# Kernel tuning notes

Hardware: AMD Instinct MI355X
Metric: run time of the kernel (lower is better)

## Reference

```python
import jax, jax.numpy as jnp
import numpy as np

HS, FF, NH = 1024, 4096, 16
HD = HS // NH
EPS = 1e-5

def _ln(x, g, b):
    m = jnp.mean(x, axis=-1, keepdims=True)
    v = jnp.mean((x - m) ** 2, axis=-1, keepdims=True)
    return (x - m) * jax.lax.rsqrt(v + EPS) * g + b

def setup_inputs() -> dict:
    key = jax.random.key(0)
    ks = jax.random.split(key, 12)
    s = 1.0 / np.sqrt(HS)
    si = 1.0 / np.sqrt(FF)
    d = {
        "hidden_states": jax.random.normal(ks[0], (2, 2048, HS), dtype=jnp.float32),
        "attention_mask": jnp.zeros((2, 1, 1, 2048), dtype=jnp.float32),
        "Wq": jax.random.uniform(ks[1], (HS, HS), minval=-s, maxval=s),
        "bq": jnp.zeros((HS,), jnp.float32),
        "Wk": jax.random.uniform(ks[2], (HS, HS), minval=-s, maxval=s),
        "bk": jnp.zeros((HS,), jnp.float32),
        "Wv": jax.random.uniform(ks[3], (HS, HS), minval=-s, maxval=s),
        "bv": jnp.zeros((HS,), jnp.float32),
        "Wo": jax.random.uniform(ks[4], (HS, HS), minval=-s, maxval=s),
        "bo": jnp.zeros((HS,), jnp.float32),
        "W1": jax.random.uniform(ks[5], (HS, FF), minval=-s, maxval=s),
        "b1": jnp.zeros((FF,), jnp.float32),
        "W2": jax.random.uniform(ks[6], (FF, HS), minval=-si, maxval=si),
        "b2": jnp.zeros((HS,), jnp.float32),
        "ln1_g": jnp.ones((HS,), jnp.float32),
        "ln1_b": jnp.zeros((HS,), jnp.float32),
        "ln2_g": jnp.ones((HS,), jnp.float32),
        "ln2_b": jnp.zeros((HS,), jnp.float32),
    }
    return d

def reference(hidden_states, attention_mask, Wq, bq, Wk, bk, Wv, bv, Wo, bo,
              W1, b1, W2, b2, ln1_g, ln1_b, ln2_g, ln2_b):
    bs, S, _ = hidden_states.shape
    x = hidden_states
    # self-attention (dropout is identity in eval)
    q = (x @ Wq + bq).reshape(bs, S, NH, HD).transpose(0, 2, 1, 3)
    k = (x @ Wk + bk).reshape(bs, S, NH, HD).transpose(0, 2, 1, 3)
    v = (x @ Wv + bv).reshape(bs, S, NH, HD).transpose(0, 2, 1, 3)
    scores = jnp.einsum("bhqd,bhkd->bhqk", q, k) / np.sqrt(HD) + attention_mask
    probs = jax.nn.softmax(scores, axis=-1)
    attn = jnp.einsum("bhqk,bhkd->bhqd", probs, v)
    attn = attn.transpose(0, 2, 1, 3).reshape(bs, S, HS)
    mha = attn @ Wo + bo
    h = _ln(x + mha, ln1_g, ln1_b)
    # FFN
    ff = jax.nn.relu(h @ W1 + b1) @ W2 + b2
    return _ln(h + ff, ln2_g, ln2_b)
```

## Files before the change

kernel.cpp:

```cpp
#include <hip/hip_runtime.h>
#include <hip/hip_bf16.h>

#define HS   1024
#define FF   4096
#define NH   16
#define HD   64
#define SEQ  2048
#define BSZ  2
#define MROWS (BSZ * SEQ)
#define EPS  1e-5f
#define QKV_STRIDE (3 * HS)

typedef float f32x4  __attribute__((ext_vector_type(4)));
typedef short bf16x8 __attribute__((ext_vector_type(8)));

__device__ __forceinline__ unsigned short f2bf(float x) {
  unsigned int u = __float_as_uint(x);
  u += 0x7fffu + ((u >> 16) & 1u);
  return (unsigned short)(u >> 16);
}

__device__ __forceinline__ unsigned int pkbf(float a, float b) {
  union { __hip_bfloat162 h; unsigned int u; } x;
  x.h = __float22bfloat162_rn(float2{a, b});
  return x.u;
}

__device__ __forceinline__ void async16(const ushort* g, ushort* lds) {
  __builtin_amdgcn_global_load_lds(
      (const __attribute__((address_space(1))) unsigned int*)g,
      (__attribute__((address_space(3))) unsigned int*)lds, 16, 0, 0);
}

template <int TBM, int TBN, bool RELU, bool OUT_BF16>
__global__ __launch_bounds__(256) void gemm_bf16_kernel(
    const ushort* __restrict__ A, const ushort* __restrict__ Bt,
    const float* __restrict__ bias, void* __restrict__ Cout,
    int M, int N, int K)
{
  constexpr int MI = TBM / 32;
  constexpr int NJ = TBN / 32;
  __shared__ ushort As[TBM * 64];
  __shared__ ushort Bs[TBN * 64];

  const int tid = threadIdx.x;
  const int wv = tid >> 6, ln = tid & 63;
  const int bn = blockIdx.x, bm = blockIdx.y;

  const int lr = ln & 15;
  const int lg = ln >> 4;
  const int mrow_base = (wv >> 1) * (TBM / 2);
  const int ncol_base = (wv & 1) * (TBN / 2);

  f32x4 acc[MI][NJ];
#pragma unroll
  for (int i = 0; i < MI; ++i)
#pragma unroll
    for (int j = 0; j < NJ; ++j) acc[i][j] = (f32x4){0.f, 0.f, 0.f, 0.f};

  const int rr = ln >> 3, cc = ln & 7;

  for (int k0 = 0; k0 < K; k0 += 64) {
    __syncthreads();
#pragma unroll
    for (int t = 0; t < TBM / 32; ++t) {
      const int R = wv * (TBM / 4) + t * 8 + rr;
      const int c = cc ^ (R & 7);
      async16(A + (size_t)(bm * TBM + R) * K + k0 + c * 8,
              &As[(size_t)(wv * (TBM / 4) + t * 8) * 64]);
    }
#pragma unroll
    for (int t = 0; t < TBN / 32; ++t) {
      const int R = wv * (TBN / 4) + t * 8 + rr;
      const int c = cc ^ (R & 7);
      async16(Bt + (size_t)(bn * TBN + R) * K + k0 + c * 8,
              &Bs[(size_t)(wv * (TBN / 4) + t * 8) * 64]);
    }
    __syncthreads();

#pragma unroll
    for (int s = 0; s < 2; ++s) {
      bf16x8 a[MI], b[NJ];
#pragma unroll
      for (int i = 0; i < MI; ++i) {
        const int m = mrow_base + i * 16 + lr;
        a[i] = *(const bf16x8*)&As[(size_t)m * 64 + (((s * 4 + lg) ^ (m & 7)) * 8)];
      }
#pragma unroll
      for (int j = 0; j < NJ; ++j) {
        const int n = ncol_base + j * 16 + lr;
        b[j] = *(const bf16x8*)&Bs[(size_t)n * 64 + (((s * 4 + lg) ^ (n & 7)) * 8)];
      }
#pragma unroll
      for (int i = 0; i < MI; ++i)
#pragma unroll
        for (int j = 0; j < NJ; ++j)
          acc[i][j] = __builtin_amdgcn_mfma_f32_16x16x32_bf16(a[i], b[j], acc[i][j], 0, 0, 0);
    }
  }

  const int gm0 = bm * TBM + mrow_base;
  const int gn0 = bn * TBN + ncol_base;
  float bs4[NJ];
#pragma unroll
  for (int j = 0; j < NJ; ++j) bs4[j] = bias[gn0 + j * 16 + lr];

  float* Cf = (float*)Cout;
  ushort* Cb = (ushort*)Cout;
#pragma unroll
  for (int i = 0; i < MI; ++i) {
#pragma unroll
    for (int r = 0; r < 4; ++r) {
      const size_t row = (size_t)(gm0 + i * 16 + lg * 4 + r);
#pragma unroll
      for (int j = 0; j < NJ; ++j) {
        float val = acc[i][j][r] + bs4[j];
        if (RELU) val = fmaxf(val, 0.f);
        const size_t idx = row * N + gn0 + j * 16 + lr;
        if (OUT_BF16) Cb[idx] = f2bf(val);
        else          Cf[idx] = val;
      }
    }
  }
}

__global__ __launch_bounds__(256) void transpose_bf16_kernel(
    const float* __restrict__ W, ushort* __restrict__ Wt, int K, int N)
{
  __shared__ ushort T[64][72];
  const int tid = threadIdx.x;
  const int n0 = blockIdx.x * 64, k0 = blockIdx.y * 64;
#pragma unroll
  for (int t = 0; t < 4; ++t) {
    const int r = t * 16 + (tid >> 4);
    const int c = (tid & 15) * 4;
    const float4 w = *(const float4*)&W[(size_t)(k0 + r) * N + n0 + c];
    T[c + 0][r] = f2bf(w.x); T[c + 1][r] = f2bf(w.y);
    T[c + 2][r] = f2bf(w.z); T[c + 3][r] = f2bf(w.w);
  }
  __syncthreads();
#pragma unroll
  for (int t = 0; t < 4; ++t) {
    const int n = t * 16 + (tid >> 4);
    const int kc = (tid & 15) * 4;
    ushort4 o;
    o.x = T[n][kc]; o.y = T[n][kc + 1]; o.z = T[n][kc + 2]; o.w = T[n][kc + 3];
    *(ushort4*)&Wt[(size_t)(n0 + n) * K + k0 + kc] = o;
  }
}

__global__ __launch_bounds__(256) void convert_bf16_kernel(
    const float* __restrict__ X, ushort* __restrict__ Y)
{
  const size_t i = ((size_t)blockIdx.x * 256 + threadIdx.x) * 4;
  const float4 v = *(const float4*)&X[i];
  ushort4 o;
  o.x = f2bf(v.x); o.y = f2bf(v.y); o.z = f2bf(v.z); o.w = f2bf(v.w);
  *(ushort4*)&Y[i] = o;
}

__global__ __launch_bounds__(256) void biascat_kernel(
    const float* __restrict__ bq, const float* __restrict__ bk,
    const float* __restrict__ bv, float* __restrict__ bqkv)
{
  const int i = blockIdx.x * 256 + threadIdx.x;
  const float v = (i < HS) ? bq[i] : (i < 2 * HS) ? bk[i - HS] : bv[i - 2 * HS];
  bqkv[i] = v;
}

__global__ __launch_bounds__(256) void vtrans_kernel(
    const ushort* __restrict__ vb, ushort* __restrict__ VTg, int stride)
{
  __shared__ ushort T[64][68];
  const int tid = threadIdx.x;
  const int s0 = blockIdx.x * 64;
  const int bh = blockIdx.y;
  const int b = bh >> 4, h = bh & 15;
#pragma unroll
  for (int t = 0; t < 4; ++t) {
    const int rr = t * 16 + (tid >> 4);
    const int c4 = (tid & 15) * 4;
    const ushort4 w = *(const ushort4*)&vb[(size_t)(b * SEQ + s0 + rr) * stride + h * 64 + c4];
    T[c4 + 0][rr] = w.x; T[c4 + 1][rr] = w.y;
    T[c4 + 2][rr] = w.z; T[c4 + 3][rr] = w.w;
  }
  __syncthreads();
#pragma unroll
  for (int t = 0; t < 4; ++t) {
    const int d = t * 16 + (tid >> 4);
    const int k4 = (tid & 15) * 4;
    ushort4 o;
    o.x = T[d][k4]; o.y = T[d][k4 + 1]; o.z = T[d][k4 + 2]; o.w = T[d][k4 + 3];
    *(ushort4*)&VTg[((size_t)bh * 64 + d) * SEQ + s0 + k4] = o;
  }
}

__global__ __launch_bounds__(512, 4) void attention_mfma_kernel(
    const ushort* __restrict__ Qb, const ushort* __restrict__ Kb,
    const ushort* __restrict__ VTg, const float* __restrict__ mask,
    ushort* __restrict__ O)
{
  __shared__ ushort smem[16384];
  ushort* Ks  = smem;
  ushort* VTs = smem + 4096;
  ushort* Ps  = smem + 8192;

  const int tid = threadIdx.x;
  const int wv = tid >> 6, ln = tid & 63;
  const int c = ln & 15, g = ln >> 4;
  const int qt = blockIdx.x, hh = blockIdx.y, b = blockIdx.z;
  const int bh = b * NH + hh;
  const size_t row0 = (size_t)b * SEQ + (size_t)qt * 128;
  const int ch = hh * HD;
  const int wq0 = wv * 16;

  bf16x8 qf[2];
#pragma unroll
  for (int s = 0; s < 2; ++s)
    qf[s] = *(const bf16x8*)&Qb[(row0 + wq0 + c) * QKV_STRIDE + ch + s * 32 + g * 8];

  f32x4 ao[4];
#pragma unroll
  for (int i = 0; i < 4; ++i) ao[i] = (f32x4){0, 0, 0, 0};
  float m_r = -1e30f, l_r = 0.f;

  ushort* Pw = Ps + wv * 1024;
  const int rr = ln >> 3, cc = ln & 7;

  for (int kb = 0; kb < SEQ / 64; ++kb) {
    __syncthreads();
    const size_t krow0 = (size_t)b * SEQ + (size_t)kb * 64;
    if (wv < 4) {
#pragma unroll
      for (int t = 0; t < 2; ++t) {
        const int r = (wv & 3) * 16 + t * 8 + rr;
        async16(Kb + (krow0 + r) * QKV_STRIDE + ch + ((cc ^ (r & 7)) * 8),
                &Ks[(size_t)((wv & 3) * 16 + t * 8) * 64]);
      }
    } else {
#pragma unroll
      for (int t = 0; t < 2; ++t) {
        const int r = (wv & 3) * 16 + t * 8 + rr;
        async16(VTg + ((size_t)bh * 64 + r) * SEQ + kb * 64 + ((cc ^ (r & 7)) * 8),
                &VTs[(size_t)((wv & 3) * 16 + t * 8) * 64]);
      }
    }
    __syncthreads();

    f32x4 as_[4];
#pragma unroll
    for (int i = 0; i < 4; ++i) as_[i] = (f32x4){0, 0, 0, 0};
#pragma unroll
    for (int s = 0; s < 2; ++s) {
#pragma unroll
      for (int mt = 0; mt < 4; ++mt) {
        const bf16x8 kf = *(const bf16x8*)&Ks[(size_t)(mt * 16 + c) * 64 + (((s * 4 + g) ^ (c & 7)) * 8)];
        as_[mt] = __builtin_amdgcn_mfma_f32_16x16x32_bf16(kf, qf[s], as_[mt], 0, 0, 0);
      }
    }

#pragma unroll
    for (int mt = 0; mt < 4; ++mt) {
      const float4 mk = *(const float4*)&mask[(size_t)b * SEQ + kb * 64 + mt * 16 + g * 4];
      as_[mt][0] = as_[mt][0] * 0.125f + mk.x;
      as_[mt][1] = as_[mt][1] * 0.125f + mk.y;
      as_[mt][2] = as_[mt][2] * 0.125f + mk.z;
      as_[mt][3] = as_[mt][3] * 0.125f + mk.w;
    }

    {
      float mx = -1e30f;
#pragma unroll
      for (int mt = 0; mt < 4; ++mt)
#pragma unroll
        for (int r = 0; r < 4; ++r) mx = fmaxf(mx, as_[mt][r]);
      mx = fmaxf(mx, __shfl_xor(mx, 16, 64));
      mx = fmaxf(mx, __shfl_xor(mx, 32, 64));
      const float nm = fmaxf(m_r, mx);
      const float alpha = __expf(m_r - nm);
      m_r = nm;
      float sum = 0.f;
#pragma unroll
      for (int mt = 0; mt < 4; ++mt)
#pragma unroll
        for (int r = 0; r < 4; ++r) {
          const float p = __expf(as_[mt][r] - nm);
          as_[mt][r] = p;
          sum += p;
        }
      sum += __shfl_xor(sum, 16, 64);
      sum += __shfl_xor(sum, 32, 64);
      l_r = l_r * alpha + sum;
#pragma unroll
      for (int mt = 0; mt < 4; ++mt)
#pragma unroll
        for (int r = 0; r < 4; ++r) ao[mt][r] *= alpha;
    }

#pragma unroll
    for (int mt = 0; mt < 4; ++mt) {
      const int q = c;
      const int kc = 2 * mt + (g >> 1);
      const int base = q * 64 + ((kc ^ (q & 7)) * 8) + 4 * (g & 1);
      *(unsigned int*)&Pw[base]     = pkbf(as_[mt][0], as_[mt][1]);
      *(unsigned int*)&Pw[base + 2] = pkbf(as_[mt][2], as_[mt][3]);
    }

#pragma unroll
    for (int s = 0; s < 2; ++s) {
      const bf16x8 pf = *(const bf16x8*)&Pw[(size_t)c * 64 + (((s * 4 + g) ^ (c & 7)) * 8)];
#pragma unroll
      for (int mt = 0; mt < 4; ++mt) {
        const bf16x8 vf = *(const bf16x8*)&VTs[(size_t)(mt * 16 + c) * 64 + (((s * 4 + g) ^ (c & 7)) * 8)];
        ao[mt] = __builtin_amdgcn_mfma_f32_16x16x32_bf16(vf, pf, ao[mt], 0, 0, 0);
      }
    }
  }

  __syncthreads();
  ushort* OL = smem;
  {
    const float inv = 1.f / l_r;
    const int q = wq0 + c;
#pragma unroll
    for (int mt = 0; mt < 4; ++mt) {
      const int d = mt * 16 + g * 4;
      uint2 w;
      w.x = pkbf(ao[mt][0] * inv, ao[mt][1] * inv);
      w.y = pkbf(ao[mt][2] * inv, ao[mt][3] * inv);
      *(uint2*)&OL[q * 72 + d] = w;
    }
  }
  __syncthreads();
#pragma unroll
  for (int it = 0; it < 2; ++it) {
    const int unit = it * 512 + tid;
    const int q = unit >> 3, sg = unit & 7;
    const uint4 w = *(const uint4*)&OL[q * 72 + sg * 8];
    *(uint4*)&O[(row0 + q) * HS + ch + sg * 8] = w;
  }
}

template <bool EMIT16>
__global__ __launch_bounds__(256) void add_ln_kernel(
    const float* __restrict__ X, const float* __restrict__ Y,
    const float* __restrict__ g, const float* __restrict__ b,
    float* __restrict__ out, ushort* __restrict__ outb)
{
  const int row = blockIdx.x;
  const int tid = threadIdx.x;
  const size_t base = (size_t)row * HS + tid * 4;
  const float4 xv = *(const float4*)&X[base];
  const float4 yv = *(const float4*)&Y[base];
  float4 v;
  v.x = xv.x + yv.x; v.y = xv.y + yv.y;
  v.z = xv.z + yv.z; v.w = xv.w + yv.w;
  float s1 = v.x + v.y + v.z + v.w;
  float s2 = v.x * v.x + v.y * v.y + v.z * v.z + v.w * v.w;
#pragma unroll
  for (int off = 32; off > 0; off >>= 1) {
    s1 += __shfl_down(s1, off, 64);
    s2 += __shfl_down(s2, off, 64);
  }
  __shared__ float red[8];
  __shared__ float stat[2];
  const int wid = tid >> 6;
  if ((tid & 63) == 0) { red[wid] = s1; red[4 + wid] = s2; }
  __syncthreads();
  if (tid == 0) {
    const float t1 = red[0] + red[1] + red[2] + red[3];
    const float t2 = red[4] + red[5] + red[6] + red[7];
    const float mean = t1 * (1.f / HS);
    const float var = t2 * (1.f / HS) - mean * mean;
    stat[0] = mean;
    stat[1] = rsqrtf(var + EPS);
  }
  __syncthreads();
  const float mean = stat[0], rstd = stat[1];
  const float4 gv = *(const float4*)&g[tid * 4];
  const float4 bv = *(const float4*)&b[tid * 4];
  float4 r;
  r.x = (v.x - mean) * rstd * gv.x + bv.x;
  r.y = (v.y - mean) * rstd * gv.y + bv.y;
  r.z = (v.z - mean) * rstd * gv.z + bv.z;
  r.w = (v.w - mean) * rstd * gv.w + bv.w;
  *(float4*)&out[base] = r;
  if (EMIT16) {
    ushort4 o;
    o.x = f2bf(r.x); o.y = f2bf(r.y); o.z = f2bf(r.z); o.w = f2bf(r.w);
    *(ushort4*)&outb[base] = o;
  }
}

extern "C" void kernel_launch(void* const* d_in, const int* in_sizes, int n_in,
                              void* d_out, int out_size, void* d_ws, size_t ws_size,
                              hipStream_t stream)
{
  const float* x    = (const float*)d_in[0];
  const float* mask = (const float*)d_in[1];
  const float* Wq   = (const float*)d_in[2];  const float* bq  = (const float*)d_in[3];
  const float* Wk   = (const float*)d_in[4];  const float* bk  = (const float*)d_in[5];
  const float* Wv   = (const float*)d_in[6];  const float* bv  = (const float*)d_in[7];
  const float* Wo   = (const float*)d_in[8];  const float* bo  = (const float*)d_in[9];
  const float* W1   = (const float*)d_in[10]; const float* b1  = (const float*)d_in[11];
  const float* W2   = (const float*)d_in[12]; const float* b2  = (const float*)d_in[13];
  const float* g1   = (const float*)d_in[14]; const float* be1 = (const float*)d_in[15];
  const float* g2   = (const float*)d_in[16]; const float* be2 = (const float*)d_in[17];
  float* out = (float*)d_out;

  ushort* wsu = (ushort*)d_ws;
  const size_t M1 = 1024 * 1024;

  ushort* Wqkvt = wsu;
  ushort* Wot   = wsu + 3 * M1;
  ushort* W1t   = wsu + 4 * M1;
  ushort* W2t   = wsu + 8 * M1;
  float*  bqkv  = (float*)(wsu + 12 * M1);
  ushort* xb    = wsu + 13 * M1;
  ushort* qkvb  = wsu + 17 * M1;
  ushort* VTg   = wsu + 29 * M1;
  ushort* attnb = wsu + 33 * M1;
  float*  mha   = (float*)(wsu + 37 * M1);
  float*  h     = (float*)(wsu + 13 * M1);
  ushort* hb    = wsu + 21 * M1;
  ushort* ff1o  = wsu + 29 * M1;
  float*  ff2o  = (float*)(wsu + 21 * M1);

  const dim3 blk(256);

  transpose_bf16_kernel<<<dim3(16, 16), blk, 0, stream>>>(Wq, Wqkvt, HS, HS);
  transpose_bf16_kernel<<<dim3(16, 16), blk, 0, stream>>>(Wk, Wqkvt + 1 * M1, HS, HS);
  transpose_bf16_kernel<<<dim3(16, 16), blk, 0, stream>>>(Wv, Wqkvt + 2 * M1, HS, HS);
  transpose_bf16_kernel<<<dim3(16, 16), blk, 0, stream>>>(Wo, Wot, HS, HS);
  transpose_bf16_kernel<<<dim3(FF / 64, HS / 64), blk, 0, stream>>>(W1, W1t, HS, FF);
  transpose_bf16_kernel<<<dim3(HS / 64, FF / 64), blk, 0, stream>>>(W2, W2t, FF, HS);
  biascat_kernel<<<dim3(12), blk, 0, stream>>>(bq, bk, bv, bqkv);

  convert_bf16_kernel<<<dim3(MROWS * HS / 1024), blk, 0, stream>>>(x, xb);

  gemm_bf16_kernel<128, 128, false, true><<<dim3(24, 32), blk, 0, stream>>>(
      xb, Wqkvt, bqkv, qkvb, MROWS, 3 * HS, HS);

  vtrans_kernel<<<dim3(SEQ / 64, BSZ * NH), blk, 0, stream>>>(qkvb + 2 * HS, VTg, QKV_STRIDE);

  attention_mfma_kernel<<<dim3(SEQ / 128, NH, BSZ), dim3(512), 0, stream>>>(
      qkvb, qkvb + HS, VTg, mask, attnb);

  gemm_bf16_kernel<64, 128, false, false><<<dim3(8, 64), blk, 0, stream>>>(
      attnb, Wot, bo, mha, MROWS, HS, HS);
  add_ln_kernel<true><<<dim3(MROWS), blk, 0, stream>>>(x, mha, g1, be1, h, hb);

  gemm_bf16_kernel<128, 128, true, true><<<dim3(32, 32), blk, 0, stream>>>(
      hb, W1t, b1, ff1o, MROWS, FF, HS);
  gemm_bf16_kernel<64, 128, false, false><<<dim3(8, 64), blk, 0, stream>>>(
      ff1o, W2t, b2, ff2o, MROWS, HS, FF);

  add_ln_kernel<false><<<dim3(MROWS), blk, 0, stream>>>(h, ff2o, g2, be2, out, nullptr);
}
```

Baseline: 405.8 us.

## Split-K output GEMMs, fuse prep kernels, widen attention key block

Several unrelated changes land together. The Wo and W2 GEMMs now use 2-way split-K, writing fp32 partial slabs that the add+LayerNorm kernel sums together with the bias, which doubles the number of blocks on the narrow N=1024 GEMMs. The weight transposes, the input conversion and the bias concat are merged into one prep launch to cut launch overhead. The attention kernel now processes 128 keys per iteration instead of 64, with larger LDS buffers, so it syncs half as often and each wave issues more MFMAs. In exchange there is extra partial-sum memory traffic, and the doubled LDS may reduce attention occupancy.

```diff
diff --git a/kernel.cpp b/kernel.cpp
--- a/kernel.cpp
+++ b/kernel.cpp
@@ -32,11 +32,11 @@
       (__attribute__((address_space(3))) unsigned int*)lds, 16, 0, 0);
 }
 
-template <int TBM, int TBN, bool RELU, bool OUT_BF16>
+template <int TBM, int TBN, bool RELU, bool OUT_BF16, bool PARTIAL>
 __global__ __launch_bounds__(256) void gemm_bf16_kernel(
     const ushort* __restrict__ A, const ushort* __restrict__ Bt,
     const float* __restrict__ bias, void* __restrict__ Cout,
-    int M, int N, int K)
+    int M, int N, int K, int kLen, size_t zstride)
 {
   constexpr int MI = TBM / 32;
   constexpr int NJ = TBN / 32;
@@ -59,8 +59,9 @@
     for (int j = 0; j < NJ; ++j) acc[i][j] = (f32x4){0.f, 0.f, 0.f, 0.f};
 
   const int rr = ln >> 3, cc = ln & 7;
-
-  for (int k0 = 0; k0 < K; k0 += 64) {
+  const int kBeg = blockIdx.z * kLen, kEnd = kBeg + kLen;
+
+  for (int k0 = kBeg; k0 < kEnd; k0 += 64) {
     __syncthreads();
 #pragma unroll
     for (int t = 0; t < TBM / 32; ++t) {
@@ -101,35 +102,46 @@
 
   const int gm0 = bm * TBM + mrow_base;
   const int gn0 = bn * TBN + ncol_base;
-  float bs4[NJ];
-#pragma unroll
-  for (int j = 0; j < NJ; ++j) bs4[j] = bias[gn0 + j * 16 + lr];
-
-  float* Cf = (float*)Cout;
-  ushort* Cb = (ushort*)Cout;
-#pragma unroll
-  for (int i = 0; i < MI; ++i) {
-#pragma unroll
-    for (int r = 0; r < 4; ++r) {
-      const size_t row = (size_t)(gm0 + i * 16 + lg * 4 + r);
-#pragma unroll
-      for (int j = 0; j < NJ; ++j) {
-        float val = acc[i][j][r] + bs4[j];
-        if (RELU) val = fmaxf(val, 0.f);
-        const size_t idx = row * N + gn0 + j * 16 + lr;
-        if (OUT_BF16) Cb[idx] = f2bf(val);
-        else          Cf[idx] = val;
+
+  if (PARTIAL) {
+    float* Cp = (float*)Cout + (size_t)blockIdx.z * zstride;
+#pragma unroll
+    for (int i = 0; i < MI; ++i)
+#pragma unroll
+      for (int r = 0; r < 4; ++r) {
+        const size_t row = (size_t)(gm0 + i * 16 + lg * 4 + r);
+#pragma unroll
+        for (int j = 0; j < NJ; ++j)
+          Cp[row * N + gn0 + j * 16 + lr] = acc[i][j][r];
       }
-    }
-  }
-}
-
-__global__ __launch_bounds__(256) void transpose_bf16_kernel(
-    const float* __restrict__ W, ushort* __restrict__ Wt, int K, int N)
-{
-  __shared__ ushort T[64][72];
-  const int tid = threadIdx.x;
-  const int n0 = blockIdx.x * 64, k0 = blockIdx.y * 64;
+  } else {
+    float bs4[NJ];
+#pragma unroll
+    for (int j = 0; j < NJ; ++j) bs4[j] = bias[gn0 + j * 16 + lr];
+    float* Cf = (float*)Cout;
+    ushort* Cb = (ushort*)Cout;
+#pragma unroll
+    for (int i = 0; i < MI; ++i) {
+#pragma unroll
+      for (int r = 0; r < 4; ++r) {
+        const size_t row = (size_t)(gm0 + i * 16 + lg * 4 + r);
+#pragma unroll
+        for (int j = 0; j < NJ; ++j) {
+          float val = acc[i][j][r] + bs4[j];
+          if (RELU) val = fmaxf(val, 0.f);
+          const size_t idx = row * N + gn0 + j * 16 + lr;
+          if (OUT_BF16) Cb[idx] = f2bf(val);
+          else          Cf[idx] = val;
+        }
+      }
+    }
+  }
+}
+
+__device__ __forceinline__ void transpose_tile(
+    const float* __restrict__ W, ushort* __restrict__ Wt,
+    int K, int N, int n0, int k0, int tid, ushort (*T)[72])
+{
 #pragma unroll
   for (int t = 0; t < 4; ++t) {
     const int r = t * 16 + (tid >> 4);
@@ -149,23 +161,47 @@
   }
 }
 
-__global__ __launch_bounds__(256) void convert_bf16_kernel(
-    const float* __restrict__ X, ushort* __restrict__ Y)
-{
-  const size_t i = ((size_t)blockIdx.x * 256 + threadIdx.x) * 4;
-  const float4 v = *(const float4*)&X[i];
-  ushort4 o;
-  o.x = f2bf(v.x); o.y = f2bf(v.y); o.z = f2bf(v.z); o.w = f2bf(v.w);
-  *(ushort4*)&Y[i] = o;
-}
-
-__global__ __launch_bounds__(256) void biascat_kernel(
+__global__ __launch_bounds__(256) void prep_kernel(
+    const float* __restrict__ Wq, const float* __restrict__ Wk,
+    const float* __restrict__ Wv, const float* __restrict__ Wo,
+    const float* __restrict__ W1, const float* __restrict__ W2,
     const float* __restrict__ bq, const float* __restrict__ bk,
-    const float* __restrict__ bv, float* __restrict__ bqkv)
-{
-  const int i = blockIdx.x * 256 + threadIdx.x;
-  const float v = (i < HS) ? bq[i] : (i < 2 * HS) ? bk[i - HS] : bv[i - 2 * HS];
-  bqkv[i] = v;
+    const float* __restrict__ bv, const float* __restrict__ x,
+    ushort* __restrict__ Wqkvt, ushort* __restrict__ Wot,
+    ushort* __restrict__ W1t, ushort* __restrict__ W2t,
+    float* __restrict__ bqkv, ushort* __restrict__ xb)
+{
+  __shared__ ushort T[64][72];
+  const int b = blockIdx.x, tid = threadIdx.x;
+  const size_t M1 = 1024 * 1024;
+  if (b < 1024) {
+    const int w = b >> 8, l = b & 255;
+    const int n0 = (l & 15) * 64, k0 = (l >> 4) * 64;
+    const float* src = (w == 0) ? Wq : (w == 1) ? Wk : (w == 2) ? Wv : Wo;
+    ushort* dst = (w < 3) ? (Wqkvt + (size_t)w * M1) : Wot;
+    transpose_tile(src, dst, HS, HS, n0, k0, tid, T);
+  } else if (b < 2048) {
+    const int l = b - 1024;
+    transpose_tile(W1, W1t, HS, FF, (l & 63) * 64, (l >> 6) * 64, tid, T);
+  } else if (b < 3072) {
+    const int l = b - 2048;
+    transpose_tile(W2, W2t, FF, HS, (l & 15) * 64, (l >> 4) * 64, tid, T);
+  } else if (b < 5120) {
+    const size_t base = (size_t)(b - 3072) * 2048 + tid * 8;
+    const float4 v0 = *(const float4*)&x[base];
+    const float4 v1 = *(const float4*)&x[base + 4];
+    ushort4 o0, o1;
+    o0.x = f2bf(v0.x); o0.y = f2bf(v0.y); o0.z = f2bf(v0.z); o0.w = f2bf(v0.w);
+    o1.x = f2bf(v1.x); o1.y = f2bf(v1.y); o1.z = f2bf(v1.z); o1.w = f2bf(v1.w);
+    *(ushort4*)&xb[base] = o0;
+    *(ushort4*)&xb[base + 4] = o1;
+  } else {
+#pragma unroll
+    for (int t = 0; t < 12; ++t) {
+      const int i = t * 256 + tid;
+      bqkv[i] = (i < HS) ? bq[i] : (i < 2 * HS) ? bk[i - HS] : bv[i - 2 * HS];
+    }
+  }
 }
 
 __global__ __launch_bounds__(256) void vtrans_kernel(
@@ -200,10 +236,10 @@
     const ushort* __restrict__ VTg, const float* __restrict__ mask,
     ushort* __restrict__ O)
 {
-  __shared__ ushort smem[16384];
+  __shared__ ushort smem[32768];
   ushort* Ks  = smem;
-  ushort* VTs = smem + 4096;
-  ushort* Ps  = smem + 8192;
+  ushort* VTs = smem + 8192;
+  ushort* Ps  = smem + 16384;
 
   const int tid = threadIdx.x;
   const int wv = tid >> 6, ln = tid & 63;
@@ -224,44 +260,44 @@
   for (int i = 0; i < 4; ++i) ao[i] = (f32x4){0, 0, 0, 0};
   float m_r = -1e30f, l_r = 0.f;
 
-  ushort* Pw = Ps + wv * 1024;
+  ushort* Pw = Ps + wv * 2048;
   const int rr = ln >> 3, cc = ln & 7;
-
-  for (int kb = 0; kb < SEQ / 64; ++kb) {
+  const int r4 = ln >> 4, sc = ln & 15;
+
+  for (int kb = 0; kb < SEQ / 128; ++kb) {
     __syncthreads();
-    const size_t krow0 = (size_t)b * SEQ + (size_t)kb * 64;
-    if (wv < 4) {
-#pragma unroll
-      for (int t = 0; t < 2; ++t) {
-        const int r = (wv & 3) * 16 + t * 8 + rr;
-        async16(Kb + (krow0 + r) * QKV_STRIDE + ch + ((cc ^ (r & 7)) * 8),
-                &Ks[(size_t)((wv & 3) * 16 + t * 8) * 64]);
-      }
-    } else {
-#pragma unroll
-      for (int t = 0; t < 2; ++t) {
-        const int r = (wv & 3) * 16 + t * 8 + rr;
-        async16(VTg + ((size_t)bh * 64 + r) * SEQ + kb * 64 + ((cc ^ (r & 7)) * 8),
-                &VTs[(size_t)((wv & 3) * 16 + t * 8) * 64]);
-      }
+    const size_t krow0 = (size_t)b * SEQ + (size_t)kb * 128;
+#pragma unroll
+    for (int t = 0; t < 2; ++t) {
+      const int r = wv * 16 + t * 8 + rr;
+      async16(Kb + (krow0 + r) * QKV_STRIDE + ch + ((cc ^ (r & 7)) * 8),
+              &Ks[(size_t)(wv * 16 + t * 8) * 64]);
+    }
+#pragma unroll
+    for (int t = 0; t < 2; ++t) {
+      const int d = wv * 8 + t * 4 + r4;
+      const int srcc = (sc & 8) | ((sc & 7) ^ (d & 7));
+      async16(VTg + ((size_t)bh * 64 + d) * SEQ + kb * 128 + srcc * 8,
+              &VTs[(size_t)(wv * 8 + t * 4) * 128]);
     }
     __syncthreads();
 
-    f32x4 as_[4];
-#pragma unroll
-    for (int i = 0; i < 4; ++i) as_[i] = (f32x4){0, 0, 0, 0};
+    f32x4 as_[8];
+#pragma unroll
+    for (int i = 0; i < 8; ++i) as_[i] = (f32x4){0, 0, 0, 0};
 #pragma unroll
     for (int s = 0; s < 2; ++s) {
 #pragma unroll
-      for (int mt = 0; mt < 4; ++mt) {
-        const bf16x8 kf = *(const bf16x8*)&Ks[(size_t)(mt * 16 + c) * 64 + (((s * 4 + g) ^ (c & 7)) * 8)];
+      for (int mt = 0; mt < 8; ++mt) {
+        const int key = mt * 16 + c;
+        const bf16x8 kf = *(const bf16x8*)&Ks[(size_t)key * 64 + (((s * 4 + g) ^ (key & 7)) * 8)];
         as_[mt] = __builtin_amdgcn_mfma_f32_16x16x32_bf16(kf, qf[s], as_[mt], 0, 0, 0);
       }
     }
 
 #pragma unroll
-    for (int mt = 0; mt < 4; ++mt) {
-      const float4 mk = *(const float4*)&mask[(size_t)b * SEQ + kb * 64 + mt * 16 + g * 4];
+    for (int mt = 0; mt < 8; ++mt) {
+      const float4 mk = *(const float4*)&mask[(size_t)b * SEQ + kb * 128 + mt * 16 + g * 4];
       as_[mt][0] = as_[mt][0] * 0.125f + mk.x;
       as_[mt][1] = as_[mt][1] * 0.125f + mk.y;
       as_[mt][2] = as_[mt][2] * 0.125f + mk.z;
@@ -271,7 +307,7 @@
     {
       float mx = -1e30f;
 #pragma unroll
-      for (int mt = 0; mt < 4; ++mt)
+      for (int mt = 0; mt < 8; ++mt)
 #pragma unroll
         for (int r = 0; r < 4; ++r) mx = fmaxf(mx, as_[mt][r]);
       mx = fmaxf(mx, __shfl_xor(mx, 16, 64));
@@ -281,7 +317,7 @@
       m_r = nm;
       float sum = 0.f;
 #pragma unroll
-      for (int mt = 0; mt < 4; ++mt)
+      for (int mt = 0; mt < 8; ++mt)
 #pragma unroll
         for (int r = 0; r < 4; ++r) {
           const float p = __expf(as_[mt][r] - nm);
@@ -298,20 +334,24 @@
     }
 
 #pragma unroll
-    for (int mt = 0; mt < 4; ++mt) {
-      const int q = c;
+    for (int mt = 0; mt < 8; ++mt) {
       const int kc = 2 * mt + (g >> 1);
-      const int base = q * 64 + ((kc ^ (q & 7)) * 8) + 4 * (g & 1);
+      const int slot = (kc & 8) | ((kc & 7) ^ (c & 7));
+      const int base = c * 128 + slot * 8 + 4 * (g & 1);
       *(unsigned int*)&Pw[base]     = pkbf(as_[mt][0], as_[mt][1]);
       *(unsigned int*)&Pw[base + 2] = pkbf(as_[mt][2], as_[mt][3]);
     }
 
 #pragma unroll
-    for (int s = 0; s < 2; ++s) {
-      const bf16x8 pf = *(const bf16x8*)&Pw[(size_t)c * 64 + (((s * 4 + g) ^ (c & 7)) * 8)];
+    for (int s = 0; s < 4; ++s) {
+      const int k = s * 4 + g;
+      const int pslot = (k & 8) | ((k & 7) ^ (c & 7));
+      const bf16x8 pf = *(const bf16x8*)&Pw[(size_t)c * 128 + pslot * 8];
 #pragma unroll
       for (int mt = 0; mt < 4; ++mt) {
-        const bf16x8 vf = *(const bf16x8*)&VTs[(size_t)(mt * 16 + c) * 64 + (((s * 4 + g) ^ (c & 7)) * 8)];
+        const int d = mt * 16 + c;
+        const int vslot = (k & 8) | ((k & 7) ^ (d & 7));
+        const bf16x8 vf = *(const bf16x8*)&VTs[(size_t)d * 128 + vslot * 8];
         ao[mt] = __builtin_amdgcn_mfma_f32_16x16x32_bf16(vf, pf, ao[mt], 0, 0, 0);
       }
     }
@@ -342,19 +382,24 @@
 }
 
 template <bool EMIT16>
-__global__ __launch_bounds__(256) void add_ln_kernel(
-    const float* __restrict__ X, const float* __restrict__ Y,
+__global__ __launch_bounds__(256) void add_ln_red_kernel(
+    const float* __restrict__ P0, const float* __restrict__ P1,
+    const float* __restrict__ bias, const float* __restrict__ X,
     const float* __restrict__ g, const float* __restrict__ b,
     float* __restrict__ out, ushort* __restrict__ outb)
 {
   const int row = blockIdx.x;
   const int tid = threadIdx.x;
   const size_t base = (size_t)row * HS + tid * 4;
+  const float4 p0 = *(const float4*)&P0[base];
+  const float4 p1 = *(const float4*)&P1[base];
+  const float4 bi = *(const float4*)&bias[tid * 4];
   const float4 xv = *(const float4*)&X[base];
-  const float4 yv = *(const float4*)&Y[base];
   float4 v;
-  v.x = xv.x + yv.x; v.y = xv.y + yv.y;
-  v.z = xv.z + yv.z; v.w = xv.w + yv.w;
+  v.x = xv.x + p0.x + p1.x + bi.x;
+  v.y = xv.y + p0.y + p1.y + bi.y;
+  v.z = xv.z + p0.z + p1.z + bi.z;
+  v.w = xv.w + p0.w + p1.w + bi.w;
   float s1 = v.x + v.y + v.z + v.w;
   float s2 = v.x * v.x + v.y * v.y + v.z * v.z + v.w * v.w;
 #pragma unroll
@@ -420,40 +465,37 @@
   ushort* qkvb  = wsu + 17 * M1;
   ushort* VTg   = wsu + 29 * M1;
   ushort* attnb = wsu + 33 * M1;
-  float*  mha   = (float*)(wsu + 37 * M1);
-  float*  h     = (float*)(wsu + 13 * M1);
-  ushort* hb    = wsu + 21 * M1;
-  ushort* ff1o  = wsu + 29 * M1;
-  float*  ff2o  = (float*)(wsu + 21 * M1);
+  float*  woP   = (float*)(wsu + 13 * M1);
+  float*  h     = (float*)(wsu + 29 * M1);
+  ushort* hb    = wsu + 37 * M1;
+  ushort* ff1o  = wsu + 13 * M1;
+  float*  ff2P0 = (float*)wsu;
+  float*  ff2P1 = (float*)(wsu + 39 * M1);
 
   const dim3 blk(256);
-
-  transpose_bf16_kernel<<<dim3(16, 16), blk, 0, stream>>>(Wq, Wqkvt, HS, HS);
-  transpose_bf16_kernel<<<dim3(16, 16), blk, 0, stream>>>(Wk, Wqkvt + 1 * M1, HS, HS);
-  transpose_bf16_kernel<<<dim3(16, 16), blk, 0, stream>>>(Wv, Wqkvt + 2 * M1, HS, HS);
-  transpose_bf16_kernel<<<dim3(16, 16), blk, 0, stream>>>(Wo, Wot, HS, HS);
-  transpose_bf16_kernel<<<dim3(FF / 64, HS / 64), blk, 0, stream>>>(W1, W1t, HS, FF);
-  transpose_bf16_kernel<<<dim3(HS / 64, FF / 64), blk, 0, stream>>>(W2, W2t, FF, HS);
-  biascat_kernel<<<dim3(12), blk, 0, stream>>>(bq, bk, bv, bqkv);
-
-  convert_bf16_kernel<<<dim3(MROWS * HS / 1024), blk, 0, stream>>>(x, xb);
-
-  gemm_bf16_kernel<128, 128, false, true><<<dim3(24, 32), blk, 0, stream>>>(
-      xb, Wqkvt, bqkv, qkvb, MROWS, 3 * HS, HS);
+  const size_t SLAB = (size_t)MROWS * HS;
+
+  prep_kernel<<<dim3(5121), blk, 0, stream>>>(
+      Wq, Wk, Wv, Wo, W1, W2, bq, bk, bv, x,
+      Wqkvt, Wot, W1t, W2t, bqkv, xb);
+
+  gemm_bf16_kernel<128, 128, false, true, false><<<dim3(24, 32), blk, 0, stream>>>(
+      xb, Wqkvt, bqkv, qkvb, MROWS, 3 * HS, HS, HS, 0);
 
   vtrans_kernel<<<dim3(SEQ / 64, BSZ * NH), blk, 0, stream>>>(qkvb + 2 * HS, VTg, QKV_STRIDE);
 
   attention_mfma_kernel<<<dim3(SEQ / 128, NH, BSZ), dim3(512), 0, stream>>>(
       qkvb, qkvb + HS, VTg, mask, attnb);
 
-  gemm_bf16_kernel<64, 128, false, false><<<dim3(8, 64), blk, 0, stream>>>(
-      attnb, Wot, bo, mha, MROWS, HS, HS);
-  add_ln_kernel<true><<<dim3(MROWS), blk, 0, stream>>>(x, mha, g1, be1, h, hb);
-
-  gemm_bf16_kernel<128, 128, true, true><<<dim3(32, 32), blk, 0, stream>>>(
-      hb, W1t, b1, ff1o, MROWS, FF, HS);
-  gemm_bf16_kernel<64, 128, false, false><<<dim3(8, 64), blk, 0, stream>>>(
-      ff1o, W2t, b2, ff2o, MROWS, HS, FF);
-
-  add_ln_kernel<false><<<dim3(MROWS), blk, 0, stream>>>(h, ff2o, g2, be2, out, nullptr);
-}
+  gemm_bf16_kernel<64, 128, false, false, true><<<dim3(8, 64, 2), blk, 0, stream>>>(
+      attnb, Wot, nullptr, woP, MROWS, HS, HS, HS / 2, SLAB);
+  add_ln_red_kernel<true><<<dim3(MROWS), blk, 0, stream>>>(
+      woP, woP + SLAB, bo, x, g1, be1, h, hb);
+
+  gemm_bf16_kernel<128, 128, true, true, false><<<dim3(32, 32), blk, 0, stream>>>(
+      hb, W1t, b1, ff1o, MROWS, FF, HS, HS, 0);
+  gemm_bf16_kernel<64, 128, false, false, true><<<dim3(8, 64, 2), blk, 0, stream>>>(
+      ff1o, W2t, nullptr, ff2P0, MROWS, HS, FF, FF / 2, (size_t)(ff2P1 - ff2P0));
+  add_ln_red_kernel<false><<<dim3(MROWS), blk, 0, stream>>>(
+      ff2P0, ff2P1, b2, h, g2, be2, out, nullptr);
+}
```

Result: no change. 398.7 us (-1.8%).
